# Kernel optimization log

Hardware: AMD Instinct MI355X
Metric: run time of the kernel (lower is better)

Reference implementation:

```python
import jax, jax.numpy as jnp
import numpy as np

B, T, C = 2, 2048, 2048
H, D, G = 16, 128, 4   # num_heads, head_dim, num_kv_groups
EPS = 1e-6


def setup_inputs() -> dict:
    key = jax.random.key(0)
    ks = jax.random.split(key, 6)
    x = jax.random.normal(ks[0], (B, T, C), dtype=jnp.float32)
    # causal mask: True = disallowed (strictly upper triangular)
    mask = jnp.triu(jnp.ones((T, T), dtype=bool), k=1)
    # RoPE tables, full head_dim with duplicated angle halves
    inv_freq = 1.0 / (10000.0 ** (jnp.arange(0, D, 2, dtype=jnp.float32) / D))
    angles = jnp.arange(T, dtype=jnp.float32)[:, None] * inv_freq[None, :]  # [T, D/2]
    angles = jnp.concatenate([angles, angles], axis=-1)                     # [T, D]
    cos, sin = jnp.cos(angles), jnp.sin(angles)
    std = 0.02
    W_query = jax.random.normal(ks[1], (C, H * D), dtype=jnp.float32) * std
    W_key = jax.random.normal(ks[2], (C, G * D), dtype=jnp.float32) * std
    W_value = jax.random.normal(ks[3], (C, G * D), dtype=jnp.float32) * std
    W_out = jax.random.normal(ks[4], (H * D, C), dtype=jnp.float32) * std
    q_scale = jnp.ones((D,), dtype=jnp.float32)
    k_scale = jnp.ones((D,), dtype=jnp.float32)
    return {"x": x, "mask": mask, "cos": cos, "sin": sin,
            "W_query": W_query, "W_key": W_key, "W_value": W_value,
            "W_out": W_out, "q_scale": q_scale, "k_scale": k_scale}


def _rmsnorm(x, scale):
    # qwen3-compatible: compute in fp32, rescale, cast back
    xf = x.astype(jnp.float32)
    var = jnp.mean(xf * xf, axis=-1, keepdims=True)
    return (xf * jax.lax.rsqrt(var + EPS) * scale).astype(x.dtype)


def _rope(x, cos, sin):
    d = x.shape[-1]
    x1, x2 = x[..., : d // 2], x[..., d // 2 :]
    rotated = jnp.concatenate([-x2, x1], axis=-1)
    # cos/sin: [T, D] -> broadcast over [B, H, T, D]
    return (x * cos[None, None] + rotated * sin[None, None]).astype(x.dtype)


def reference(x, mask, cos, sin, W_query, W_key, W_value, W_out, q_scale, k_scale):
    b, t, _ = x.shape
    Q = (x @ W_query).reshape(b, t, H, D).transpose(0, 2, 1, 3)  # [B,H,T,D]
    K = (x @ W_key).reshape(b, t, G, D).transpose(0, 2, 1, 3)    # [B,G,T,D]
    V = (x @ W_value).reshape(b, t, G, D).transpose(0, 2, 1, 3)
    group_size = H // G
    K = jnp.repeat(K, group_size, axis=1)  # [B,H,T,D]
    V = jnp.repeat(V, group_size, axis=1)
    Q = _rmsnorm(Q, q_scale)
    K = _rmsnorm(K, k_scale)
    Q = _rope(Q, cos, sin)
    K = _rope(K, cos, sin)
    scale = D ** (-0.5)
    attn = jnp.einsum("bhqd,bhkd->bhqk", Q, K) * scale
    attn = jnp.where(mask[None, None], -jnp.inf, attn)
    w = jax.nn.softmax(attn, axis=-1)
    out = jnp.einsum("bhqk,bhkd->bhqd", w, V)
    out = out.transpose(0, 2, 1, 3).reshape(b, t, H * D)
    return out @ W_out
```

## Files before the change

### kernel.cpp

```cpp
#include <hip/hip_runtime.h>
#include <hip/hip_bf16.h>

#define Bq 2
#define Tt 2048
#define Cc 2048
#define Hh 16
#define Dd 128
#define Gg 4

using bf16 = __hip_bfloat16;
typedef __attribute__((ext_vector_type(8))) short short8;
typedef __attribute__((ext_vector_type(4))) float f32x4;

__device__ __forceinline__ void gload_lds16(const void* g, void* l) {
    __builtin_amdgcn_global_load_lds(
        (const __attribute__((address_space(1))) unsigned int*)g,
        (__attribute__((address_space(3))) unsigned int*)l, 16, 0, 0);
}

__global__ void k_cast_bf16(const float* __restrict__ in, bf16* __restrict__ out, int n4) {
    int i = blockIdx.x * blockDim.x + threadIdx.x;
    if (i >= n4) return;
    float4 v = ((const float4*)in)[i];
    union { bf16 h[4]; uint2 u; } u;
    u.h[0] = __float2bfloat16(v.x);
    u.h[1] = __float2bfloat16(v.y);
    u.h[2] = __float2bfloat16(v.z);
    u.h[3] = __float2bfloat16(v.w);
    ((uint2*)out)[i] = u.u;
}

__global__ void k_cast_transpose(const float* __restrict__ in, bf16* __restrict__ out,
                                 int rows, int cols, int ostride) {
    __shared__ float tile[32][33];
    int c0 = blockIdx.x * 32, r0 = blockIdx.y * 32;
    int tx = threadIdx.x, ty = threadIdx.y;
    #pragma unroll
    for (int k = 0; k < 4; ++k)
        tile[ty + 8*k][tx] = in[(size_t)(r0 + ty + 8*k) * cols + c0 + tx];
    __syncthreads();
    #pragma unroll
    for (int k = 0; k < 4; ++k)
        out[(size_t)(c0 + ty + 8*k) * ostride + r0 + tx] = __float2bfloat16(tile[tx][ty + 8*k]);
}

__global__ void k_vt(const bf16* __restrict__ QKV, bf16* __restrict__ Vt) {
    __shared__ bf16 tile[64][65];
    const int d0 = blockIdx.x * 64, t0 = blockIdx.y * 64;
    const int bg = blockIdx.z;
    const int b = bg >> 2, g = bg & 3;
    const int tx = threadIdx.x, ty = threadIdx.y;
    const bf16* src = QKV + (size_t)(b * Tt) * 3072 + 2560 + g * 128;
    #pragma unroll
    for (int k = 0; k < 8; ++k)
        tile[ty + 8*k][tx] = src[(size_t)(t0 + ty + 8*k) * 3072 + d0 + tx];
    __syncthreads();
    bf16* dst = Vt + (size_t)bg * Dd * Tt;
    #pragma unroll
    for (int k = 0; k < 8; ++k)
        dst[(size_t)(d0 + ty + 8*k) * Tt + t0 + tx] = tile[tx][ty + 8*k];
}

template<int OUTF32>
__global__ __launch_bounds__(256)
void k_gemm_bt(const bf16* __restrict__ A, const bf16* __restrict__ Bt,
               void* __restrict__ C, int M, int N, int K) {
    __shared__ __align__(16) bf16 As[128 * 64];
    __shared__ __align__(16) bf16 Bs[128 * 64];
    const int lane = threadIdx.x & 63;
    const int wave = threadIdx.x >> 6;
    const int row0 = blockIdx.y * 128;
    const int col0 = blockIdx.x * 128;
    const int wm = wave >> 1, wn = wave & 1;
    f32x4 acc[4][4] = {};

    const int srow = lane >> 3;
    const int schunk = ((lane & 7) ^ srow) * 8;

    for (int k0 = 0; k0 < K; k0 += 64) {
        #pragma unroll
        for (int j = 0; j < 4; ++j) {
            const int c = j * 4 + wave;
            const int rt = c * 8 + srow;
            gload_lds16(A  + (size_t)(row0 + rt) * K + k0 + schunk, As + c * 512);
            gload_lds16(Bt + (size_t)(col0 + rt) * K + k0 + schunk, Bs + c * 512);
        }
        __syncthreads();
        #pragma unroll
        for (int kk = 0; kk < 2; ++kk) {
            short8 af[4], bfr[4];
            #pragma unroll
            for (int i = 0; i < 4; ++i) {
                const int ra = wm * 64 + i * 16 + (lane & 15);
                af[i] = *(const short8*)((const char*)As + ra * 128 +
                        ((kk * 64 + (lane >> 4) * 16) ^ ((ra & 7) << 4)));
                const int rb = wn * 64 + i * 16 + (lane & 15);
                bfr[i] = *(const short8*)((const char*)Bs + rb * 128 +
                        ((kk * 64 + (lane >> 4) * 16) ^ ((rb & 7) << 4)));
            }
            __builtin_amdgcn_s_setprio(1);
            #pragma unroll
            for (int i = 0; i < 4; ++i)
                #pragma unroll
                for (int j = 0; j < 4; ++j)
                    acc[i][j] = __builtin_amdgcn_mfma_f32_16x16x32_bf16(af[i], bfr[j], acc[i][j], 0, 0, 0);
            __builtin_amdgcn_s_setprio(0);
        }
        __syncthreads();
    }

    const int crow0 = row0 + wm * 64 + (lane >> 4) * 4;
    const int ccol0 = col0 + wn * 64 + (lane & 15);
    #pragma unroll
    for (int i = 0; i < 4; ++i)
        #pragma unroll
        for (int j = 0; j < 4; ++j)
            #pragma unroll
            for (int r = 0; r < 4; ++r) {
                const size_t idx = (size_t)(crow0 + i * 16 + r) * N + ccol0 + j * 16;
                const float v = acc[i][j][r];
                if (OUTF32) ((float*)C)[idx] = v;
                else        ((bf16*)C)[idx] = __float2bfloat16(v);
            }
}

__global__ void k_qkv_post(const bf16* __restrict__ QKV,
                           const float* __restrict__ cosT, const float* __restrict__ sinT,
                           const float* __restrict__ qs, const float* __restrict__ ks,
                           bf16* __restrict__ Qr, bf16* __restrict__ Kr) {
    const int bt = blockIdx.x;
    const int b = bt >> 11;
    const int t = bt & 2047;
    const int lane = threadIdx.x & 63;
    const int wave = threadIdx.x >> 6;
    const float c1 = cosT[t * 128 + lane],      c2 = cosT[t * 128 + 64 + lane];
    const float s1 = sinT[t * 128 + lane],      s2 = sinT[t * 128 + 64 + lane];
    const float qs1 = qs[lane], qs2 = qs[lane + 64];
    const float ks1 = ks[lane], ks2 = ks[lane + 64];
    const bf16* rowb = QKV + (size_t)bt * 3072;
    for (int rr = wave; rr < 20; rr += 4) {
        const bf16* src = rowb + rr * 128;
        const float x1 = __bfloat162float(src[lane]);
        const float x2 = __bfloat162float(src[lane + 64]);
        bf16* dst;
        if (rr < 16) dst = Qr + ((size_t)(b * Hh + rr) * Tt + t) * 128;
        else         dst = Kr + ((size_t)(b * Gg + (rr - 16)) * Tt + t) * 128;
        float ssum = x1 * x1 + x2 * x2;
        #pragma unroll
        for (int o = 32; o > 0; o >>= 1) ssum += __shfl_xor(ssum, o);
        const float inv = rsqrtf(ssum * (1.0f / 128.0f) + 1e-6f);
        const float sc1 = (rr < 16) ? qs1 : ks1;
        const float sc2 = (rr < 16) ? qs2 : ks2;
        const float y1 = x1 * inv * sc1;
        const float y2 = x2 * inv * sc2;
        dst[lane]      = __float2bfloat16(y1 * c1 - y2 * s1);
        dst[lane + 64] = __float2bfloat16(y2 * c2 + y1 * s2);
    }
}

__global__ __launch_bounds__(256)
void k_attn(const bf16* __restrict__ Qr, const bf16* __restrict__ Kr,
            const bf16* __restrict__ Vt, bf16* __restrict__ AO) {
    __shared__ __align__(16) bf16 Ksm[64 * 128];
    __shared__ __align__(16) bf16 Vsm[128 * 64];
    __shared__ __align__(16) bf16 Psm[4][16 * 64];
    const int id = blockIdx.x;
    const int bg = id & 7;
    const int wid = id >> 3;
    const int pair = wid & 15;
    const int hg = wid >> 4;
    const int b = bg >> 2, g = bg & 3;
    const int h = g * 4 + hg;
    const int lane = threadIdx.x & 63;
    const int wave = threadIdx.x >> 6;

    const bf16* Kbase = Kr + (size_t)(b * Gg + g) * Tt * Dd;
    const bf16* Vbase = Vt + (size_t)(b * Gg + g) * Dd * Tt;

    for (int pass = 0; pass < 2; ++pass) {
        const int qt = pass ? (31 - pair) : pair;
        const bf16* Qbase = Qr + ((size_t)(b * Hh + h) * Tt + qt * 64) * Dd;

        short8 qf[4];
        #pragma unroll
        for (int kk = 0; kk < 4; ++kk)
            qf[kk] = *(const short8*)(Qbase + (size_t)(wave * 16 + (lane & 15)) * 128 + kk * 32 + (lane >> 4) * 8);

        float m_run[4], l_run[4];
        f32x4 oacc[8];
        #pragma unroll
        for (int r = 0; r < 4; ++r) { m_run[r] = -1e30f; l_run[r] = 0.f; }
        #pragma unroll
        for (int j = 0; j < 8; ++j) oacc[j] = (f32x4){0.f, 0.f, 0.f, 0.f};

        for (int tk = 0; tk <= qt; ++tk) {
            const int k0 = tk * 64;
            #pragma unroll
            for (int j = 0; j < 4; ++j) {
                const int c = j * 4 + wave;
                const int rt = c * 4 + (lane >> 4);
                const int chunk = (lane & 15) ^ (rt & 7);
                gload_lds16(Kbase + (size_t)(k0 + rt) * 128 + chunk * 8, Ksm + c * 512);
            }
            #pragma unroll
            for (int j = 0; j < 4; ++j) {
                const int c = j * 4 + wave;
                const int rt = c * 8 + (lane >> 3);
                const int chunk = (lane & 7) ^ ((lane >> 3) & 7);
                gload_lds16(Vbase + (size_t)rt * Tt + k0 + chunk * 8, Vsm + c * 512);
            }
            __syncthreads();

            f32x4 s[4];
            #pragma unroll
            for (int nt = 0; nt < 4; ++nt) s[nt] = (f32x4){0.f, 0.f, 0.f, 0.f};
            __builtin_amdgcn_s_setprio(1);
            #pragma unroll
            for (int nt = 0; nt < 4; ++nt) {
                #pragma unroll
                for (int kk = 0; kk < 4; ++kk) {
                    const int rk = nt * 16 + (lane & 15);
                    short8 kf = *(const short8*)((const char*)Ksm + rk * 256 +
                                ((kk * 64 + (lane >> 4) * 16) ^ ((rk & 7) << 4)));
                    s[nt] = __builtin_amdgcn_mfma_f32_16x16x32_bf16(qf[kk], kf, s[nt], 0, 0, 0);
                }
            }
            __builtin_amdgcn_s_setprio(0);

            const int qrow = qt * 64 + wave * 16 + (lane >> 4) * 4;
            #pragma unroll
            for (int nt = 0; nt < 4; ++nt) {
                const int kcol = k0 + nt * 16 + (lane & 15);
                #pragma unroll
                for (int r = 0; r < 4; ++r) {
                    const float v = s[nt][r] * 0.08838834764831845f;
                    s[nt][r] = (kcol > qrow + r) ? -1e30f : v;
                }
            }
            float tm[4];
            #pragma unroll
            for (int r = 0; r < 4; ++r)
                tm[r] = fmaxf(fmaxf(s[0][r], s[1][r]), fmaxf(s[2][r], s[3][r]));
            #pragma unroll
            for (int o = 1; o < 16; o <<= 1)
                #pragma unroll
                for (int r = 0; r < 4; ++r) tm[r] = fmaxf(tm[r], __shfl_xor(tm[r], o));
            float fsc[4], ts[4];
            #pragma unroll
            for (int r = 0; r < 4; ++r) {
                const float mn = fmaxf(m_run[r], tm[r]);
                fsc[r] = __expf(m_run[r] - mn);
                m_run[r] = mn;
                l_run[r] *= fsc[r];
                ts[r] = 0.f;
            }
            #pragma unroll
            for (int j = 0; j < 8; ++j)
                #pragma unroll
                for (int r = 0; r < 4; ++r) oacc[j][r] *= fsc[r];
            #pragma unroll
            for (int nt = 0; nt < 4; ++nt)
                #pragma unroll
                for (int r = 0; r < 4; ++r) {
                    const float p = __expf(s[nt][r] - m_run[r]);
                    ts[r] += p;
                    s[nt][r] = p;
                }
            #pragma unroll
            for (int o = 1; o < 16; o <<= 1)
                #pragma unroll
                for (int r = 0; r < 4; ++r) ts[r] += __shfl_xor(ts[r], o);
            #pragma unroll
            for (int r = 0; r < 4; ++r) l_run[r] += ts[r];

            #pragma unroll
            for (int nt = 0; nt < 4; ++nt)
                #pragma unroll
                for (int r = 0; r < 4; ++r) {
                    const int prow = (lane >> 4) * 4 + r;
                    const int pcol = nt * 16 + (lane & 15);
                    *(bf16*)((char*)Psm[wave] + ((prow * 128 + pcol * 2) ^ ((prow & 7) << 4))) =
                        __float2bfloat16(s[nt][r]);
                }
            #pragma unroll
            for (int kk = 0; kk < 2; ++kk) {
                const int pr = lane & 15;
                short8 pf = *(const short8*)((const char*)Psm[wave] + pr * 128 +
                            ((kk * 64 + (lane >> 4) * 16) ^ ((pr & 7) << 4)));
                __builtin_amdgcn_s_setprio(1);
                #pragma unroll
                for (int j = 0; j < 8; ++j) {
                    const int rb = j * 16 + (lane & 15);
                    short8 vf = *(const short8*)((const char*)Vsm + rb * 128 +
                                ((kk * 64 + (lane >> 4) * 16) ^ ((rb & 7) << 4)));
                    oacc[j] = __builtin_amdgcn_mfma_f32_16x16x32_bf16(pf, vf, oacc[j], 0, 0, 0);
                }
                __builtin_amdgcn_s_setprio(0);
            }
            __syncthreads();
        }

        #pragma unroll
        for (int r = 0; r < 4; ++r) {
            const float inv = 1.0f / l_run[r];
            const int qrow = qt * 64 + wave * 16 + (lane >> 4) * 4 + r;
            bf16* dst = AO + (size_t)(b * Tt + qrow) * 2048 + h * 128 + (lane & 15);
            #pragma unroll
            for (int j = 0; j < 8; ++j)
                dst[j * 16] = __float2bfloat16(oacc[j][r] * inv);
        }
    }
}

extern "C" void kernel_launch(void* const* d_in, const int* in_sizes, int n_in,
                              void* d_out, int out_size, void* d_ws, size_t ws_size,
                              hipStream_t stream) {
    const float* x    = (const float*)d_in[0];
    const float* cosT = (const float*)d_in[2];
    const float* sinT = (const float*)d_in[3];
    const float* Wq   = (const float*)d_in[4];
    const float* Wk   = (const float*)d_in[5];
    const float* Wv   = (const float*)d_in[6];
    const float* Wo   = (const float*)d_in[7];
    const float* qs   = (const float*)d_in[8];
    const float* ks   = (const float*)d_in[9];

    char* ws = (char*)d_ws;
    bf16* xb   = (bf16*)(ws);
    bf16* Wcat = (bf16*)(ws + 16777216);
    bf16* Wot  = (bf16*)(ws + 29360128);
    bf16* QKV  = (bf16*)(ws + 37748736);
    bf16* Qr   = (bf16*)(ws + 62914560);
    bf16* Kr   = (bf16*)(ws + 79691776);
    bf16* Vtp  = (bf16*)(ws + 83886080);
    bf16* AO   = (bf16*)(ws + 88080384);

    k_cast_bf16<<<8192, 256, 0, stream>>>(x, xb, 2097152);
    dim3 tb(32, 8);
    k_cast_transpose<<<dim3(64, 64), tb, 0, stream>>>(Wq, Wcat, 2048, 2048, 2048);
    k_cast_transpose<<<dim3(16, 64), tb, 0, stream>>>(Wk, Wcat + (size_t)2048 * 2048, 2048, 512, 2048);
    k_cast_transpose<<<dim3(16, 64), tb, 0, stream>>>(Wv, Wcat + (size_t)2560 * 2048, 2048, 512, 2048);
    k_cast_transpose<<<dim3(64, 64), tb, 0, stream>>>(Wo, Wot, 2048, 2048, 2048);

    k_gemm_bt<0><<<dim3(24, 32), 256, 0, stream>>>(xb, Wcat, QKV, 4096, 3072, 2048);
    k_qkv_post<<<4096, 256, 0, stream>>>(QKV, cosT, sinT, qs, ks, Qr, Kr);
    k_vt<<<dim3(2, 32, 8), dim3(64, 8), 0, stream>>>(QKV, Vtp);
    k_attn<<<512, 256, 0, stream>>>(Qr, Kr, Vtp, AO);
    k_gemm_bt<1><<<dim3(16, 32), 256, 0, stream>>>(AO, Wot, d_out, 4096, 2048, 2048);
}
```

Baseline: 228.7 us.

## Double-buffer K/V tiles in attention, fold softmax scale into Q, lazy rescale

Result: no change. 225.6 us (-1.3%).

```diff
diff --git a/kernel.cpp b/kernel.cpp
--- a/kernel.cpp
+++ b/kernel.cpp
@@ -149,20 +149,21 @@
         #pragma unroll
         for (int o = 32; o > 0; o >>= 1) ssum += __shfl_xor(ssum, o);
         const float inv = rsqrtf(ssum * (1.0f / 128.0f) + 1e-6f);
-        const float sc1 = (rr < 16) ? qs1 : ks1;
-        const float sc2 = (rr < 16) ? qs2 : ks2;
-        const float y1 = x1 * inv * sc1;
-        const float y2 = x2 * inv * sc2;
-        dst[lane]      = __float2bfloat16(y1 * c1 - y2 * s1);
-        dst[lane + 64] = __float2bfloat16(y2 * c2 + y1 * s2);
+        const float post = (rr < 16) ? 0.08838834764831845f : 1.0f;
+        const float sc1 = ((rr < 16) ? qs1 : ks1) * inv;
+        const float sc2 = ((rr < 16) ? qs2 : ks2) * inv;
+        const float y1 = x1 * sc1;
+        const float y2 = x2 * sc2;
+        dst[lane]      = __float2bfloat16((y1 * c1 - y2 * s1) * post);
+        dst[lane + 64] = __float2bfloat16((y2 * c2 + y1 * s2) * post);
     }
 }
 
 __global__ __launch_bounds__(256)
 void k_attn(const bf16* __restrict__ Qr, const bf16* __restrict__ Kr,
             const bf16* __restrict__ Vt, bf16* __restrict__ AO) {
-    __shared__ __align__(16) bf16 Ksm[64 * 128];
-    __shared__ __align__(16) bf16 Vsm[128 * 64];
+    __shared__ __align__(16) bf16 Ksm[2][64 * 128];
+    __shared__ __align__(16) bf16 Vsm[2][128 * 64];
     __shared__ __align__(16) bf16 Psm[4][16 * 64];
     const int id = blockIdx.x;
     const int bg = id & 7;
@@ -193,23 +194,40 @@
         #pragma unroll
         for (int j = 0; j < 8; ++j) oacc[j] = (f32x4){0.f, 0.f, 0.f, 0.f};
 
-        for (int tk = 0; tk <= qt; ++tk) {
-            const int k0 = tk * 64;
+        {
+            const int k0 = 0;
             #pragma unroll
             for (int j = 0; j < 4; ++j) {
                 const int c = j * 4 + wave;
-                const int rt = c * 4 + (lane >> 4);
-                const int chunk = (lane & 15) ^ (rt & 7);
-                gload_lds16(Kbase + (size_t)(k0 + rt) * 128 + chunk * 8, Ksm + c * 512);
-            }
-            #pragma unroll
-            for (int j = 0; j < 4; ++j) {
-                const int c = j * 4 + wave;
-                const int rt = c * 8 + (lane >> 3);
-                const int chunk = (lane & 7) ^ ((lane >> 3) & 7);
-                gload_lds16(Vbase + (size_t)rt * Tt + k0 + chunk * 8, Vsm + c * 512);
-            }
+                const int rtk = c * 4 + (lane >> 4);
+                const int chk = (lane & 15) ^ (rtk & 7);
+                gload_lds16(Kbase + (size_t)(k0 + rtk) * 128 + chk * 8, Ksm[0] + c * 512);
+                const int rtv = c * 8 + (lane >> 3);
+                const int chv = (lane & 7) ^ ((lane >> 3) & 7);
+                gload_lds16(Vbase + (size_t)rtv * Tt + k0 + chv * 8, Vsm[0] + c * 512);
+            }
+        }
+
+        int cur = 0;
+        for (int tk = 0; tk <= qt; ++tk) {
             __syncthreads();
+
+            if (tk < qt) {
+                const int k0n = (tk + 1) * 64;
+                #pragma unroll
+                for (int j = 0; j < 4; ++j) {
+                    const int c = j * 4 + wave;
+                    const int rtk = c * 4 + (lane >> 4);
+                    const int chk = (lane & 15) ^ (rtk & 7);
+                    gload_lds16(Kbase + (size_t)(k0n + rtk) * 128 + chk * 8, Ksm[cur ^ 1] + c * 512);
+                    const int rtv = c * 8 + (lane >> 3);
+                    const int chv = (lane & 7) ^ ((lane >> 3) & 7);
+                    gload_lds16(Vbase + (size_t)rtv * Tt + k0n + chv * 8, Vsm[cur ^ 1] + c * 512);
+                }
+            }
+
+            const bf16* Ks = Ksm[cur];
+            const bf16* Vs = Vsm[cur];
 
             f32x4 s[4];
             #pragma unroll
@@ -220,23 +238,25 @@
                 #pragma unroll
                 for (int kk = 0; kk < 4; ++kk) {
                     const int rk = nt * 16 + (lane & 15);
-                    short8 kf = *(const short8*)((const char*)Ksm + rk * 256 +
+                    short8 kf = *(const short8*)((const char*)Ks + rk * 256 +
                                 ((kk * 64 + (lane >> 4) * 16) ^ ((rk & 7) << 4)));
                     s[nt] = __builtin_amdgcn_mfma_f32_16x16x32_bf16(qf[kk], kf, s[nt], 0, 0, 0);
                 }
             }
             __builtin_amdgcn_s_setprio(0);
 
-            const int qrow = qt * 64 + wave * 16 + (lane >> 4) * 4;
-            #pragma unroll
-            for (int nt = 0; nt < 4; ++nt) {
-                const int kcol = k0 + nt * 16 + (lane & 15);
-                #pragma unroll
-                for (int r = 0; r < 4; ++r) {
-                    const float v = s[nt][r] * 0.08838834764831845f;
-                    s[nt][r] = (kcol > qrow + r) ? -1e30f : v;
-                }
-            }
+            if (tk == qt) {
+                const int qrow = qt * 64 + wave * 16 + (lane >> 4) * 4;
+                const int k0 = tk * 64;
+                #pragma unroll
+                for (int nt = 0; nt < 4; ++nt) {
+                    const int kcol = k0 + nt * 16 + (lane & 15);
+                    #pragma unroll
+                    for (int r = 0; r < 4; ++r)
+                        if (kcol > qrow + r) s[nt][r] = -1e30f;
+                }
+            }
+
             float tm[4];
             #pragma unroll
             for (int r = 0; r < 4; ++r)
@@ -245,19 +265,26 @@
             for (int o = 1; o < 16; o <<= 1)
                 #pragma unroll
                 for (int r = 0; r < 4; ++r) tm[r] = fmaxf(tm[r], __shfl_xor(tm[r], o));
-            float fsc[4], ts[4];
-            #pragma unroll
-            for (int r = 0; r < 4; ++r) {
-                const float mn = fmaxf(m_run[r], tm[r]);
-                fsc[r] = __expf(m_run[r] - mn);
-                m_run[r] = mn;
-                l_run[r] *= fsc[r];
-                ts[r] = 0.f;
-            }
-            #pragma unroll
-            for (int j = 0; j < 8; ++j)
-                #pragma unroll
-                for (int r = 0; r < 4; ++r) oacc[j][r] *= fsc[r];
+
+            bool ok = true;
+            #pragma unroll
+            for (int r = 0; r < 4; ++r) ok = ok && (tm[r] <= m_run[r] + 8.0f);
+            if (!__all(ok)) {
+                float fsc[4];
+                #pragma unroll
+                for (int r = 0; r < 4; ++r) {
+                    const float mn = fmaxf(m_run[r], tm[r]);
+                    fsc[r] = __expf(m_run[r] - mn);
+                    m_run[r] = mn;
+                    l_run[r] *= fsc[r];
+                }
+                #pragma unroll
+                for (int j = 0; j < 8; ++j)
+                    #pragma unroll
+                    for (int r = 0; r < 4; ++r) oacc[j][r] *= fsc[r];
+            }
+
+            float ts[4] = {0.f, 0.f, 0.f, 0.f};
             #pragma unroll
             for (int nt = 0; nt < 4; ++nt)
                 #pragma unroll
@@ -291,14 +318,15 @@
                 #pragma unroll
                 for (int j = 0; j < 8; ++j) {
                     const int rb = j * 16 + (lane & 15);
-                    short8 vf = *(const short8*)((const char*)Vsm + rb * 128 +
+                    short8 vf = *(const short8*)((const char*)Vs + rb * 128 +
                                 ((kk * 64 + (lane >> 4) * 16) ^ ((rb & 7) << 4)));
                     oacc[j] = __builtin_amdgcn_mfma_f32_16x16x32_bf16(pf, vf, oacc[j], 0, 0, 0);
                 }
                 __builtin_amdgcn_s_setprio(0);
             }
-            __syncthreads();
-        }
+            cur ^= 1;
+        }
+        __syncthreads();
 
         #pragma unroll
         for (int r = 0; r < 4; ++r) {
```
